# Performance work log

Measured on AMD Instinct MI355X. Metric: run time of the kernel, lower is better.

The kernel has to match this reference:

```python
import jax, jax.numpy as jnp
import numpy as np

EPS = 1e-6  # torch.nn.PairwiseDistance default eps, added to the difference before norm
B, D, H, W = 2048, 1024, 128, 128


def setup_inputs() -> dict:
    key = jax.random.key(0)
    k1, k2 = jax.random.split(key)
    x = jax.random.normal(k1, (B, D), dtype=jnp.float32)
    # SOM codebook: [input_size, H*W], matches torch.randn(input_size, out_size[0]*out_size[1])
    weight = jax.random.normal(k2, (D, H * W), dtype=jnp.float32)
    # grid locations, row-major (x, y) as produced by get_map_index()
    gx, gy = jnp.meshgrid(jnp.arange(H), jnp.arange(W), indexing='ij')
    locations = jnp.stack([gx.ravel(), gy.ravel()], axis=1).astype(jnp.float32)  # [H*W, 2]
    return {"x": x, "weight": weight, "locations": locations}


def reference(x, weight, locations):
    # dists[b, m] = || x[b] - weight[:, m] + EPS ||_2  (PairwiseDistance p=2 semantics)
    d = x.shape[1]
    sq = (jnp.sum(x * x, axis=1, keepdims=True)          # [B, 1]
          + jnp.sum(weight * weight, axis=0)[None, :]    # [1, M]
          - 2.0 * (x @ weight)                            # [B, M] GEMM
          + 2.0 * EPS * (jnp.sum(x, axis=1, keepdims=True) - jnp.sum(weight, axis=0)[None, :])
          + d * EPS * EPS)
    dists = jnp.sqrt(jnp.maximum(sq, 0.0))                # [B, M]
    losses = jnp.min(dists, axis=1, keepdims=True)        # [B, 1]
    bmu_indexes = jnp.argmin(dists, axis=1, keepdims=True)  # [B, 1] int
    bmu_locations = locations[bmu_indexes]                 # [B, 1, 2]
    loss = jnp.sum(losses) / x.shape[0]                    # scalar mean min-distance
    return bmu_indexes, bmu_locations, loss
```

## Files before the change

kernel.cpp:

```cpp
#include <hip/hip_runtime.h>
#include <cstdint>
#include <cstddef>


#define B_  2048
#define D_  1024
#define M_  16384
#define EPS_ 1e-6f

typedef _Float16 v8h __attribute__((ext_vector_type(8)));
typedef float    v4f __attribute__((ext_vector_type(4)));

static __device__ __forceinline__ unsigned long long umin64(unsigned long long a,
                                                            unsigned long long b) {
    return a < b ? a : b;
}

static __device__ __forceinline__ size_t addr16(int r, int c) {
    return (size_t)(r >> 4) * 32768 + (size_t)(c >> 2) * 1024 +
           (size_t)(c & 3) * 256 + (size_t)(r & 15) * 16;
}

#define GLDS16(g, l)                                                            \
    __builtin_amdgcn_global_load_lds(                                           \
        (const __attribute__((address_space(1))) void*)(g),                     \
        (__attribute__((address_space(3))) void*)(l), 16, 0, 0)

__global__ __launch_bounds__(256) void prep(
    const float* __restrict__ x, const float* __restrict__ W,
    _Float16* __restrict__ xh, _Float16* __restrict__ xl,
    _Float16* __restrict__ wth, _Float16* __restrict__ wtl,
    float* __restrict__ rowTerm, float* __restrict__ colTerm,
    unsigned long long* __restrict__ keys, float* __restrict__ out)
{
    const int t = threadIdx.x;
    const int blk = blockIdx.x;
    if (blk < 2048) {
        __shared__ float cpart[4][64];
        const int mg = blk >> 3, dc = blk & 7;
        const int m_local = t & 63;
        const int wq = t >> 6;
        const int m = mg * 64 + m_local;
        const float* wp = W + m;
        float part = 0.f;
        #pragma unroll
        for (int cl = 0; cl < 4; ++cl) {
            const int c = dc * 16 + wq * 4 + cl;
            const int d0 = c * 8;
            float vv[8];
            #pragma unroll
            for (int e = 0; e < 8; ++e)
                vv[e] = wp[(size_t)(d0 + e) * M_];
            v8h h, l;
            #pragma unroll
            for (int e = 0; e < 8; ++e) {
                _Float16 hi = (_Float16)vv[e];
                h[e] = hi; l[e] = (_Float16)(vv[e] - (float)hi);
                part += vv[e] * vv[e] - 2.0f * EPS_ * vv[e];
            }
            const size_t a = addr16(m, c);
            *(v8h*)((char*)wth + a) = h;
            *(v8h*)((char*)wtl + a) = l;
        }
        cpart[wq][m_local] = part;
        __syncthreads();
        if (t < 64)
            atomicAdd(&colTerm[mg * 64 + t],
                      cpart[0][t] + cpart[1][t] + cpart[2][t] + cpart[3][t]);
    } else {
        const int xb = blk - 2048;
        const int w = t >> 6, L = t & 63;
        const int hl = L & 31;
        const int r = xb * 8 + 2 * w + (L >> 5);
        const float* xr = x + (size_t)r * D_;
        float part = 0.f;
        #pragma unroll
        for (int i = 0; i < 4; ++i) {
            const int c = 32 * i + hl;
            float4 q1 = *(const float4*)(xr + 8 * c);
            float4 q2 = *(const float4*)(xr + 8 * c + 4);
            float vv[8] = {q1.x, q1.y, q1.z, q1.w, q2.x, q2.y, q2.z, q2.w};
            v8h h, l;
            #pragma unroll
            for (int e = 0; e < 8; ++e) {
                _Float16 hi = (_Float16)vv[e];
                h[e] = hi; l[e] = (_Float16)(vv[e] - (float)hi);
                part += vv[e] * vv[e] + 2.0f * EPS_ * vv[e];
            }
            const size_t a = addr16(r, c);
            *(v8h*)((char*)xh + a) = h;
            *(v8h*)((char*)xl + a) = l;
        }
        #pragma unroll
        for (int msk = 1; msk <= 16; msk <<= 1)
            part += __shfl_xor(part, msk, 64);
        if (hl == 0) rowTerm[r] = part;
        if (xb == 0) {
            for (int i = t; i < B_; i += 256) keys[i] = ~0ull;
            if (t == 0) out[3 * B_] = 0.f;
        }
    }
}

__global__ __launch_bounds__(256, 2) void som_mfma(
    const _Float16* __restrict__ xh, const _Float16* __restrict__ xl,
    const _Float16* __restrict__ wth, const _Float16* __restrict__ wtl,
    const float* __restrict__ rowTerm, const float* __restrict__ colTerm,
    unsigned long long* __restrict__ keys)
{
    __shared__ __align__(16) char smem[49152];
    _Float16* Ah = (_Float16*)smem;
    _Float16* Al = (_Float16*)(smem + 8192);
    _Float16* Bh = (_Float16*)(smem + 16384);
    _Float16* Bl = (_Float16*)(smem + 32768);

    const int t = threadIdx.x;
    const int g = blockIdx.x;
    const int slab = (g & 7) + 8 * (g >> 7);
    const int cb = slab * 256;
    const int rb = ((g >> 3) & 15) * 128;
    const int L = t & 63, w = t >> 6;
    const int wro = (w >> 1) * 64;
    const int wco = (w & 1) * 128;
    const int c16 = L & 15, kq = L >> 4;

    const int wgrp = t >> 6;
    const int lane16 = (t & 63) * 16;
    const int ldsw = wgrp * 1024;
    const size_t abase0 = (size_t)((rb >> 4) + wgrp) * 32768 + lane16;
    const size_t abase1 = abase0 + 4ull * 32768;
    const size_t bbase0 = (size_t)((cb >> 4) + wgrp) * 32768 + lane16;
    const size_t bbase1 = bbase0 + 4ull * 32768;
    const size_t bbase2 = bbase0 + 8ull * 32768;
    const size_t bbase3 = bbase0 + 12ull * 32768;

    const char* pxh = (const char*)xh;
    const char* pxl = (const char*)xl;
    const char* pwh = (const char*)wth;
    const char* pwl = (const char*)wtl;

    v4f acc[4][8];
    #pragma unroll
    for (int i = 0; i < 4; ++i)
        #pragma unroll
        for (int j = 0; j < 8; ++j) acc[i][j] = (v4f){0.f, 0.f, 0.f, 0.f};

    const int lofs = kq * 128 + c16 * 8;
    int ia[4], ibx[8];
    #pragma unroll
    for (int i = 0; i < 4; ++i) ia[i] = ((wro >> 4) + i) * 512 + lofs;
    #pragma unroll
    for (int j = 0; j < 8; ++j) ibx[j] = ((wco >> 4) + j) * 512 + lofs;

    for (int S = 0; S < 32; ++S) {
        const size_t ko = (size_t)S * 1024;
        __syncthreads();
        GLDS16(pxh + abase0 + ko, smem + ldsw);
        GLDS16(pxh + abase1 + ko, smem + 4096 + ldsw);
        GLDS16(pxl + abase0 + ko, smem + 8192 + ldsw);
        GLDS16(pxl + abase1 + ko, smem + 12288 + ldsw);
        GLDS16(pwh + bbase0 + ko, smem + 16384 + ldsw);
        GLDS16(pwh + bbase1 + ko, smem + 20480 + ldsw);
        GLDS16(pwh + bbase2 + ko, smem + 24576 + ldsw);
        GLDS16(pwh + bbase3 + ko, smem + 28672 + ldsw);
        GLDS16(pwl + bbase0 + ko, smem + 32768 + ldsw);
        GLDS16(pwl + bbase1 + ko, smem + 36864 + ldsw);
        GLDS16(pwl + bbase2 + ko, smem + 40960 + ldsw);
        GLDS16(pwl + bbase3 + ko, smem + 45056 + ldsw);
        __syncthreads();

        v8h ah[4], al4[4], bh4[4], bl4[4];
        #pragma unroll
        for (int i = 0; i < 4; ++i) {
            ah[i]  = *(const v8h*)(Ah + ia[i]);
            al4[i] = *(const v8h*)(Al + ia[i]);
        }
        #pragma unroll
        for (int j = 0; j < 4; ++j) {
            bh4[j] = *(const v8h*)(Bh + ibx[j]);
            bl4[j] = *(const v8h*)(Bl + ibx[j]);
        }
        #pragma unroll
        for (int i = 0; i < 4; ++i)
            #pragma unroll
            for (int j = 0; j < 4; ++j) {
                acc[i][j] = __builtin_amdgcn_mfma_f32_16x16x32_f16(ah[i],  bh4[j], acc[i][j], 0, 0, 0);
                acc[i][j] = __builtin_amdgcn_mfma_f32_16x16x32_f16(ah[i],  bl4[j], acc[i][j], 0, 0, 0);
                acc[i][j] = __builtin_amdgcn_mfma_f32_16x16x32_f16(al4[i], bh4[j], acc[i][j], 0, 0, 0);
            }
        #pragma unroll
        for (int j = 0; j < 4; ++j) {
            bh4[j] = *(const v8h*)(Bh + ibx[j + 4]);
            bl4[j] = *(const v8h*)(Bl + ibx[j + 4]);
        }
        #pragma unroll
        for (int i = 0; i < 4; ++i)
            #pragma unroll
            for (int j = 0; j < 4; ++j) {
                acc[i][j+4] = __builtin_amdgcn_mfma_f32_16x16x32_f16(ah[i],  bh4[j], acc[i][j+4], 0, 0, 0);
                acc[i][j+4] = __builtin_amdgcn_mfma_f32_16x16x32_f16(ah[i],  bl4[j], acc[i][j+4], 0, 0, 0);
                acc[i][j+4] = __builtin_amdgcn_mfma_f32_16x16x32_f16(al4[i], bh4[j], acc[i][j+4], 0, 0, 0);
            }
    }

    float cT[8];
    #pragma unroll
    for (int j = 0; j < 8; ++j) cT[j] = colTerm[cb + wco + j * 16 + c16];
    const float de2 = (float)D_ * EPS_ * EPS_;
    #pragma unroll
    for (int i = 0; i < 4; ++i) {
        #pragma unroll
        for (int r = 0; r < 4; ++r) {
            int row_g = rb + wro + i * 16 + kq * 4 + r;
            float rt = rowTerm[row_g];
            unsigned long long best = ~0ull;
            #pragma unroll
            for (int j = 0; j < 8; ++j) {
                float sq = rt + cT[j] - 2.0f * acc[i][j][r] + de2;
                sq = fmaxf(sq, 0.0f);
                float dist = sqrtf(sq);
                unsigned long long key =
                    ((unsigned long long)__float_as_uint(dist) << 32) |
                    (unsigned int)(cb + wco + j * 16 + c16);
                best = umin64(best, key);
            }
            #pragma unroll
            for (int m = 1; m <= 8; m <<= 1) {
                unsigned long long o =
                    (unsigned long long)__shfl_xor((long long)best, m, 64);
                best = umin64(best, o);
            }
            if (c16 == 0) atomicMin(&keys[row_g], best);
        }
    }
}

__global__ void row_stats(const float* __restrict__ x, float* __restrict__ rowTerm) {
    int b = blockIdx.x;
    const float* xr = x + (size_t)b * D_;
    int t = threadIdx.x;
    float acc = 0.f;
    for (int i = t; i < D_; i += 256) {
        float v = xr[i];
        acc += v * v + 2.0f * EPS_ * v;
    }
    for (int off = 32; off; off >>= 1) acc += __shfl_down(acc, off, 64);
    __shared__ float s[4];
    if ((t & 63) == 0) s[t >> 6] = acc;
    __syncthreads();
    if (t == 0) rowTerm[b] = s[0] + s[1] + s[2] + s[3];
}

__global__ void col_stats(const float* __restrict__ w, float* __restrict__ colTerm) {
    int m = blockIdx.x * 256 + threadIdx.x;
    int d0 = blockIdx.y * 64;
    const float* p = w + (size_t)d0 * M_ + m;
    float acc = 0.f;
    #pragma unroll 8
    for (int d = 0; d < 64; ++d) {
        float v = p[(size_t)d * M_];
        acc += v * v - 2.0f * EPS_ * v;
    }
    atomicAdd(&colTerm[m], acc);
}

__global__ __launch_bounds__(256, 2) void som_gemm(
    const float* __restrict__ A, const float* __restrict__ Wt,
    const float* __restrict__ rowTerm, const float* __restrict__ colTerm,
    unsigned long long* __restrict__ keys)
{
    __shared__ float As[8][128];
    __shared__ float Bs[8][128];
    const int t  = threadIdx.x;
    const int rb = blockIdx.y * 128;
    const int cb = blockIdx.x * 128;
    const int tx = t & 15;
    const int ty = t >> 4;
    float acc[8][8];
    #pragma unroll
    for (int i = 0; i < 8; ++i)
        #pragma unroll
        for (int j = 0; j < 8; ++j) acc[i][j] = 0.f;
    const int la_row = t >> 1, la_k = (t & 1) * 4;
    const int lb_k = t >> 5, lb_n = (t & 31) * 4;
    const float* Aptr = A + (size_t)(rb + la_row) * D_ + la_k;
    const float* Bptr = Wt + (size_t)lb_k * M_ + cb + lb_n;
    for (int k0 = 0; k0 < D_; k0 += 8) {
        float4 av = *(const float4*)(Aptr + k0);
        float4 bv = *(const float4*)(Bptr + (size_t)k0 * M_);
        __syncthreads();
        As[la_k + 0][la_row] = av.x;
        As[la_k + 1][la_row] = av.y;
        As[la_k + 2][la_row] = av.z;
        As[la_k + 3][la_row] = av.w;
        *(float4*)&Bs[lb_k][lb_n] = bv;
        __syncthreads();
        #pragma unroll
        for (int k = 0; k < 8; ++k) {
            float a[8], b[8];
            #pragma unroll
            for (int i = 0; i < 8; ++i) a[i] = As[k][ty * 8 + i];
            #pragma unroll
            for (int j = 0; j < 8; ++j) b[j] = Bs[k][tx * 8 + j];
            #pragma unroll
            for (int i = 0; i < 8; ++i)
                #pragma unroll
                for (int j = 0; j < 8; ++j) acc[i][j] += a[i] * b[j];
        }
    }
    float rT[8], cT[8];
    #pragma unroll
    for (int i = 0; i < 8; ++i) rT[i] = rowTerm[rb + ty * 8 + i];
    #pragma unroll
    for (int j = 0; j < 8; ++j) cT[j] = colTerm[cb + tx * 8 + j];
    const float de2 = (float)D_ * EPS_ * EPS_;
    #pragma unroll
    for (int i = 0; i < 8; ++i) {
        unsigned long long best = ~0ull;
        #pragma unroll
        for (int j = 0; j < 8; ++j) {
            float sq = rT[i] + cT[j] - 2.0f * acc[i][j] + de2;
            sq = fmaxf(sq, 0.0f);
            float dist = sqrtf(sq);
            unsigned long long key =
                ((unsigned long long)__float_as_uint(dist) << 32) |
                (unsigned int)(cb + tx * 8 + j);
            best = umin64(best, key);
        }
        #pragma unroll
        for (int msk = 1; msk <= 8; msk <<= 1) {
            unsigned long long o = __shfl_xor((long long)best, msk, 64);
            best = umin64(best, (unsigned long long)o);
        }
        if (tx == 0) atomicMin(&keys[rb + ty * 8 + i], best);
    }
}

__global__ void finalize(const unsigned long long* __restrict__ keys,
                         const float* __restrict__ loc,
                         float* __restrict__ out)
{
    int t = threadIdx.x;
    int r = blockIdx.x * 256 + t;
    unsigned long long k = keys[r];
    unsigned int idx = (unsigned int)(k & 0xFFFFFFFFu);
    float dist = __uint_as_float((unsigned int)(k >> 32));
    out[r] = (float)idx;
    out[B_ + 2 * r]     = loc[2 * idx];
    out[B_ + 2 * r + 1] = loc[2 * idx + 1];
    float sum = dist;
    for (int off = 32; off; off >>= 1) sum += __shfl_down(sum, off, 64);
    __shared__ float s[4];
    if ((t & 63) == 0) s[t >> 6] = sum;
    __syncthreads();
    if (t == 0) atomicAdd(&out[3 * B_], (s[0] + s[1] + s[2] + s[3]) / (float)B_);
}

extern "C" void kernel_launch(void* const* d_in, const int* in_sizes, int n_in,
                              void* d_out, int out_size, void* d_ws, size_t ws_size,
                              hipStream_t stream)
{
    const float* x   = (const float*)d_in[0];
    const float* w   = (const float*)d_in[1];
    const float* loc = (const float*)d_in[2];
    float* out = (float*)d_out;

    char* ws = (char*)d_ws;
    unsigned long long* keys = (unsigned long long*)ws;
    float* rowTerm = (float*)(ws + (16 << 10));
    float* colTerm = (float*)(ws + (24 << 10));
    _Float16* xh  = (_Float16*)(ws + (1ull << 20));
    _Float16* xl  = (_Float16*)(ws + (5ull << 20));
    _Float16* wth = (_Float16*)(ws + (9ull << 20));
    _Float16* wtl = (_Float16*)(ws + (41ull << 20));
    const size_t NEED = 73ull << 20;

    if (ws_size >= NEED) {
        hipMemsetAsync(colTerm, 0, M_ * sizeof(float), stream);
        prep<<<2304, 256, 0, stream>>>(x, w, xh, xl, wth, wtl,
                                       rowTerm, colTerm, keys, out);
        som_mfma<<<1024, 256, 0, stream>>>(
            xh, xl, wth, wtl, rowTerm, colTerm, keys);
    } else {
        hipMemsetAsync(keys, 0xFF, B_ * sizeof(unsigned long long), stream);
        hipMemsetAsync(colTerm, 0, M_ * sizeof(float), stream);
        hipMemsetAsync(out + 3 * B_, 0, sizeof(float), stream);
        row_stats<<<B_, 256, 0, stream>>>(x, rowTerm);
        col_stats<<<dim3(M_ / 256, D_ / 64), 256, 0, stream>>>(w, colTerm);
        som_gemm<<<dim3(M_ / 128, B_ / 128), 256, 0, stream>>>(
            x, w, rowTerm, colTerm, keys);
    }
    finalize<<<8, 256, 0, stream>>>(keys, loc, out);
}
```

Measured before the change: 299.3 us.

## Double-buffer LDS tiles in MFMA GEMM and replace colTerm atomics with partials

The GEMM main loop now uses two 48KB LDS buffers, prefetching the next K-slab via global_load_lds while computing on the current one. It uses explicit vmcnt/lgkmcnt waits and raw barriers instead of two __syncthreads per step. Occupancy drops to one block per SM via launch bounds and 96KB dynamic shared memory. Separately, column-norm partials are written per D-chunk and summed in the epilogue, which removes the memset and the atomics. The trade-off is lower occupancy and more fragile hand-placed synchronization.

```diff
diff --git a/kernel.cpp b/kernel.cpp
--- a/kernel.cpp
+++ b/kernel.cpp
@@ -30,7 +30,7 @@
     const float* __restrict__ x, const float* __restrict__ W,
     _Float16* __restrict__ xh, _Float16* __restrict__ xl,
     _Float16* __restrict__ wth, _Float16* __restrict__ wtl,
-    float* __restrict__ rowTerm, float* __restrict__ colTerm,
+    float* __restrict__ rowTerm, float* __restrict__ colPart,
     unsigned long long* __restrict__ keys, float* __restrict__ out)
 {
     const int t = threadIdx.x;
@@ -65,8 +65,8 @@
         cpart[wq][m_local] = part;
         __syncthreads();
         if (t < 64)
-            atomicAdd(&colTerm[mg * 64 + t],
-                      cpart[0][t] + cpart[1][t] + cpart[2][t] + cpart[3][t]);
+            colPart[(size_t)dc * M_ + mg * 64 + t] =
+                cpart[0][t] + cpart[1][t] + cpart[2][t] + cpart[3][t];
     } else {
         const int xb = blk - 2048;
         const int w = t >> 6, L = t & 63;
@@ -102,17 +102,13 @@
     }
 }
 
-__global__ __launch_bounds__(256, 2) void som_mfma(
+__global__ __launch_bounds__(256, 1) void som_mfma(
     const _Float16* __restrict__ xh, const _Float16* __restrict__ xl,
     const _Float16* __restrict__ wth, const _Float16* __restrict__ wtl,
-    const float* __restrict__ rowTerm, const float* __restrict__ colTerm,
+    const float* __restrict__ rowTerm, const float* __restrict__ colPart,
     unsigned long long* __restrict__ keys)
 {
-    __shared__ __align__(16) char smem[49152];
-    _Float16* Ah = (_Float16*)smem;
-    _Float16* Al = (_Float16*)(smem + 8192);
-    _Float16* Bh = (_Float16*)(smem + 16384);
-    _Float16* Bl = (_Float16*)(smem + 32768);
+    extern __shared__ __align__(16) char smem[];
 
     const int t = threadIdx.x;
     const int g = blockIdx.x;
@@ -124,12 +120,11 @@
     const int wco = (w & 1) * 128;
     const int c16 = L & 15, kq = L >> 4;
 
-    const int wgrp = t >> 6;
-    const int lane16 = (t & 63) * 16;
-    const int ldsw = wgrp * 1024;
-    const size_t abase0 = (size_t)((rb >> 4) + wgrp) * 32768 + lane16;
+    const int lane16 = L * 16;
+    const int ldsw = w * 1024;
+    const size_t abase0 = (size_t)((rb >> 4) + w) * 32768 + lane16;
     const size_t abase1 = abase0 + 4ull * 32768;
-    const size_t bbase0 = (size_t)((cb >> 4) + wgrp) * 32768 + lane16;
+    const size_t bbase0 = (size_t)((cb >> 4) + w) * 32768 + lane16;
     const size_t bbase1 = bbase0 + 4ull * 32768;
     const size_t bbase2 = bbase0 + 8ull * 32768;
     const size_t bbase3 = bbase0 + 12ull * 32768;
@@ -152,24 +147,44 @@
     #pragma unroll
     for (int j = 0; j < 8; ++j) ibx[j] = ((wco >> 4) + j) * 512 + lofs;
 
+#define STAGE(S_, bsel)                                                         \
+    do {                                                                        \
+        char* _b = smem + (bsel) * 49152 + ldsw;                                \
+        const size_t _ko = (size_t)(S_) * 1024;                                 \
+        GLDS16(pxh + abase0 + _ko, _b);                                         \
+        GLDS16(pxh + abase1 + _ko, _b + 4096);                                  \
+        GLDS16(pxl + abase0 + _ko, _b + 8192);                                  \
+        GLDS16(pxl + abase1 + _ko, _b + 12288);                                 \
+        GLDS16(pwh + bbase0 + _ko, _b + 16384);                                 \
+        GLDS16(pwh + bbase1 + _ko, _b + 20480);                                 \
+        GLDS16(pwh + bbase2 + _ko, _b + 24576);                                 \
+        GLDS16(pwh + bbase3 + _ko, _b + 28672);                                 \
+        GLDS16(pwl + bbase0 + _ko, _b + 32768);                                 \
+        GLDS16(pwl + bbase1 + _ko, _b + 36864);                                 \
+        GLDS16(pwl + bbase2 + _ko, _b + 40960);                                 \
+        GLDS16(pwl + bbase3 + _ko, _b + 45056);                                 \
+    } while (0)
+
+    STAGE(0, 0);
+
     for (int S = 0; S < 32; ++S) {
-        const size_t ko = (size_t)S * 1024;
-        __syncthreads();
-        GLDS16(pxh + abase0 + ko, smem + ldsw);
-        GLDS16(pxh + abase1 + ko, smem + 4096 + ldsw);
-        GLDS16(pxl + abase0 + ko, smem + 8192 + ldsw);
-        GLDS16(pxl + abase1 + ko, smem + 12288 + ldsw);
-        GLDS16(pwh + bbase0 + ko, smem + 16384 + ldsw);
-        GLDS16(pwh + bbase1 + ko, smem + 20480 + ldsw);
-        GLDS16(pwh + bbase2 + ko, smem + 24576 + ldsw);
-        GLDS16(pwh + bbase3 + ko, smem + 28672 + ldsw);
-        GLDS16(pwl + bbase0 + ko, smem + 32768 + ldsw);
-        GLDS16(pwl + bbase1 + ko, smem + 36864 + ldsw);
-        GLDS16(pwl + bbase2 + ko, smem + 40960 + ldsw);
-        GLDS16(pwl + bbase3 + ko, smem + 45056 + ldsw);
-        __syncthreads();
-
-        v8h ah[4], al4[4], bh4[4], bl4[4];
+        const int cur = S & 1;
+        if (S < 31) {
+            STAGE(S + 1, cur ^ 1);
+            asm volatile("s_waitcnt vmcnt(12)" ::: "memory");
+        } else {
+            asm volatile("s_waitcnt vmcnt(0)" ::: "memory");
+        }
+        __builtin_amdgcn_sched_barrier(0);
+        __builtin_amdgcn_s_barrier();
+        __builtin_amdgcn_sched_barrier(0);
+
+        const _Float16* Ah = (const _Float16*)(smem + cur * 49152);
+        const _Float16* Al = (const _Float16*)(smem + cur * 49152 + 8192);
+        const _Float16* Bh = (const _Float16*)(smem + cur * 49152 + 16384);
+        const _Float16* Bl = (const _Float16*)(smem + cur * 49152 + 32768);
+
+        v8h ah[4], al4[4], bh4[4], bl4[4], bh8[4], bl8[4];
         #pragma unroll
         for (int i = 0; i < 4; ++i) {
             ah[i]  = *(const v8h*)(Ah + ia[i]);
@@ -190,22 +205,33 @@
             }
         #pragma unroll
         for (int j = 0; j < 4; ++j) {
-            bh4[j] = *(const v8h*)(Bh + ibx[j + 4]);
-            bl4[j] = *(const v8h*)(Bl + ibx[j + 4]);
-        }
+            bh8[j] = *(const v8h*)(Bh + ibx[j + 4]);
+            bl8[j] = *(const v8h*)(Bl + ibx[j + 4]);
+        }
+        asm volatile("s_waitcnt lgkmcnt(0)" ::: "memory");
+        __builtin_amdgcn_sched_barrier(0);
+        __builtin_amdgcn_s_barrier();
+        __builtin_amdgcn_sched_barrier(0);
         #pragma unroll
         for (int i = 0; i < 4; ++i)
             #pragma unroll
             for (int j = 0; j < 4; ++j) {
-                acc[i][j+4] = __builtin_amdgcn_mfma_f32_16x16x32_f16(ah[i],  bh4[j], acc[i][j+4], 0, 0, 0);
-                acc[i][j+4] = __builtin_amdgcn_mfma_f32_16x16x32_f16(ah[i],  bl4[j], acc[i][j+4], 0, 0, 0);
-                acc[i][j+4] = __builtin_amdgcn_mfma_f32_16x16x32_f16(al4[i], bh4[j], acc[i][j+4], 0, 0, 0);
-            }
-    }
+                acc[i][j+4] = __builtin_amdgcn_mfma_f32_16x16x32_f16(ah[i],  bh8[j], acc[i][j+4], 0, 0, 0);
+                acc[i][j+4] = __builtin_amdgcn_mfma_f32_16x16x32_f16(ah[i],  bl8[j], acc[i][j+4], 0, 0, 0);
+                acc[i][j+4] = __builtin_amdgcn_mfma_f32_16x16x32_f16(al4[i], bh8[j], acc[i][j+4], 0, 0, 0);
+            }
+    }
+#undef STAGE
 
     float cT[8];
     #pragma unroll
-    for (int j = 0; j < 8; ++j) cT[j] = colTerm[cb + wco + j * 16 + c16];
+    for (int j = 0; j < 8; ++j) {
+        const int col = cb + wco + j * 16 + c16;
+        float s = 0.f;
+        #pragma unroll
+        for (int p = 0; p < 8; ++p) s += colPart[(size_t)p * M_ + col];
+        cT[j] = s;
+    }
     const float de2 = (float)D_ * EPS_ * EPS_;
     #pragma unroll
     for (int i = 0; i < 4; ++i) {
@@ -368,7 +394,7 @@
     char* ws = (char*)d_ws;
     unsigned long long* keys = (unsigned long long*)ws;
     float* rowTerm = (float*)(ws + (16 << 10));
-    float* colTerm = (float*)(ws + (24 << 10));
+    float* colPart = (float*)(ws + (24 << 10));
     _Float16* xh  = (_Float16*)(ws + (1ull << 20));
     _Float16* xl  = (_Float16*)(ws + (5ull << 20));
     _Float16* wth = (_Float16*)(ws + (9ull << 20));
@@ -376,19 +402,18 @@
     const size_t NEED = 73ull << 20;
 
     if (ws_size >= NEED) {
-        hipMemsetAsync(colTerm, 0, M_ * sizeof(float), stream);
         prep<<<2304, 256, 0, stream>>>(x, w, xh, xl, wth, wtl,
-                                       rowTerm, colTerm, keys, out);
-        som_mfma<<<1024, 256, 0, stream>>>(
-            xh, xl, wth, wtl, rowTerm, colTerm, keys);
+                                       rowTerm, colPart, keys, out);
+        som_mfma<<<1024, 256, 98304, stream>>>(
+            xh, xl, wth, wtl, rowTerm, colPart, keys);
     } else {
         hipMemsetAsync(keys, 0xFF, B_ * sizeof(unsigned long long), stream);
-        hipMemsetAsync(colTerm, 0, M_ * sizeof(float), stream);
+        hipMemsetAsync(colPart, 0, M_ * sizeof(float), stream);
         hipMemsetAsync(out + 3 * B_, 0, sizeof(float), stream);
         row_stats<<<B_, 256, 0, stream>>>(x, rowTerm);
-        col_stats<<<dim3(M_ / 256, D_ / 64), 256, 0, stream>>>(w, colTerm);
+        col_stats<<<dim3(M_ / 256, D_ / 64), 256, 0, stream>>>(w, colPart);
         som_gemm<<<dim3(M_ / 128, B_ / 128), 256, 0, stream>>>(
-            x, w, rowTerm, colTerm, keys);
+            x, w, rowTerm, colPart, keys);
     }
     finalize<<<8, 256, 0, stream>>>(keys, loc, out);
 }
```

After: 378.8 us. +26.6%, slower.
